# Kernel tuning notes

Measured on AMD Instinct MI355X. Metric: run time of the kernel, lower is better.

Reference implementation:

```python
import jax, jax.numpy as jnp
import numpy as np
from jax import lax

NPOINT = 1024
FG_NSAMPLE = 512
TOPK = 2048
NSAMPLE = 32
RADIUS = 0.3
BN_EPS = 1e-5


def masked_fps(xyz, mask, n):
    """Farthest point sampling restricted to points where mask is True.
    xyz: [B,N,3] (grad-stopped), mask: [B,N] bool. Returns int32 [B,n] indices.
    Equivalent to running FPS on the masked subset starting at its first point."""
    xyz = lax.stop_gradient(xyz)

    def one(x, m):
        mind0 = jnp.where(m, jnp.float32(1e10), jnp.float32(-1.0))

        def body(i, carry):
            mind, idxs = carry
            sel = jnp.argmax(mind).astype(jnp.int32)
            d = jnp.sum((x - x[sel]) ** 2, axis=-1)
            mind = jnp.where(m, jnp.minimum(mind, d), jnp.float32(-1.0))
            return mind, idxs.at[i].set(sel)

        _, idxs = lax.fori_loop(0, n, body, (mind0, jnp.zeros((n,), jnp.int32)))
        return idxs

    return jax.vmap(one)(xyz, mask)


def ball_query(xyz, new_xyz, radius, nsample):
    """xyz: [B,N,3], new_xyz: [B,S,3] -> int32 [B,S,nsample] of first neighbors
    within radius (padded with the first found index, as in pointnet2 CUDA)."""
    x = lax.stop_gradient(xyz)
    q = lax.stop_gradient(new_xyz)
    d2 = jnp.sum((q[:, :, None, :] - x[:, None, :, :]) ** 2, axis=-1)  # [B,S,N]
    N = x.shape[1]
    ar = jnp.arange(N, dtype=jnp.float32)
    key = jnp.where(d2 <= radius * radius, ar, jnp.float32(N))
    neg_top, _ = lax.top_k(-key, nsample)  # smallest nsample indices
    idx = (-neg_top).astype(jnp.int32)
    first = idx[..., :1]
    idx = jnp.where(idx >= N, first, idx)
    return jnp.clip(idx, 0, N - 1)


def conv_bn_relu_2d(x, W, g, b):
    # x: [B,C,S,ns], W: [O,C]; 1x1 conv (no bias) + training-mode BN + ReLU
    y = jnp.einsum('oc,bcsn->bosn', W, x)
    mu = y.mean((0, 2, 3), keepdims=True)
    var = y.var((0, 2, 3), keepdims=True)
    y = (y - mu) * lax.rsqrt(var + BN_EPS) * g[None, :, None, None] + b[None, :, None, None]
    return jax.nn.relu(y)


def conv_bn_relu_1d(x, W, g, b):
    # x: [B,C,N]
    y = jnp.einsum('oc,bcn->bon', W, x)
    mu = y.mean((0, 2), keepdims=True)
    var = y.var((0, 2), keepdims=True)
    y = (y - mu) * lax.rsqrt(var + BN_EPS) * g[None, :, None] + b[None, :, None]
    return jax.nn.relu(y)


def batch_gather_points(x, idx):
    # x: [B,N,3], idx: [B,...] -> [B,...,3]
    return jax.vmap(lambda a, i: a[i])(x, idx)


def batch_gather_feats(f, idx):
    # f: [B,C,N], idx: [B,S,ns] -> [B,C,S,ns]
    return jax.vmap(lambda a, i: a[:, i])(f, idx)


def setup_inputs() -> dict:
    key = jax.random.key(0)
    ks = jax.random.split(key, 16)
    B, N, C = 4, 16384, 128
    s = 0.05
    return {
        'xyz': jax.random.uniform(ks[0], (B, N, 3), dtype=jnp.float32),
        'features': jax.random.normal(ks[1], (B, C, N), dtype=jnp.float32),
        # grouped shared MLP: (3+C)->128->128->256
        'w1': jax.random.normal(ks[2], (128, 131), dtype=jnp.float32) * s,
        'g1': jnp.ones((128,), jnp.float32), 'b1': jnp.zeros((128,), jnp.float32),
        'w2': jax.random.normal(ks[3], (128, 128), dtype=jnp.float32) * s,
        'g2': jnp.ones((128,), jnp.float32), 'b2': jnp.zeros((128,), jnp.float32),
        'w3': jax.random.normal(ks[4], (256, 128), dtype=jnp.float32) * s,
        'g3': jnp.ones((256,), jnp.float32), 'b3': jnp.zeros((256,), jnp.float32),
        # fbs mask MLP: C->64->2 (last layer plain conv with bias)
        'fw1': jax.random.normal(ks[5], (64, 128), dtype=jnp.float32) * s,
        'fg1': jnp.ones((64,), jnp.float32), 'fb1': jnp.zeros((64,), jnp.float32),
        'fw2': jax.random.normal(ks[6], (2, 64), dtype=jnp.float32) * s,
        'fbias2': jnp.zeros((2,), jnp.float32),
    }


def reference(xyz, features, w1, g1, b1, w2, g2, b2, w3, g3, b3, fw1, fg1, fb1, fw2, fbias2):
    B, N, _ = xyz.shape
    # --- FBS: foreground/background scoring ---
    h = conv_bn_relu_1d(features, fw1, fg1, fb1)                 # [B,64,N]
    mask_scores = jnp.einsum('oc,bcn->bon', fw2, h) + fbias2[None, :, None]  # [B,2,N]
    soft = jax.nn.softmax(mask_scores, axis=1)
    margin = soft[:, 1, :] - soft[:, 0, :]                        # [B,N]
    _, top_idx = lax.top_k(margin, TOPK)
    fg_mask = jnp.zeros((B, N), bool).at[jnp.arange(B)[:, None], top_idx].set(True)
    # --- mask-restricted FPS on foreground and background ---
    fg_idx = masked_fps(xyz, fg_mask, FG_NSAMPLE)                 # [B,512]
    bg_idx = masked_fps(xyz, ~fg_mask, NPOINT - FG_NSAMPLE)       # [B,512]
    indices = jnp.concatenate([fg_idx, bg_idx], axis=1)          # [B,npoint]
    new_xyz = batch_gather_points(xyz, indices)                   # [B,npoint,3]
    # --- ball query + grouping ---
    idx = ball_query(xyz, new_xyz, RADIUS, NSAMPLE)               # [B,S,ns]
    grouped_xyz = batch_gather_points(xyz, idx)                   # [B,S,ns,3]
    grouped_xyz = grouped_xyz - new_xyz[:, :, None, :]
    grouped_xyz = jnp.transpose(grouped_xyz, (0, 3, 1, 2))        # [B,3,S,ns]
    grouped_feats = batch_gather_feats(features, idx)             # [B,C,S,ns]
    x = jnp.concatenate([grouped_xyz, grouped_feats], axis=1)     # [B,3+C,S,ns]
    # --- shared MLP + max pool over neighbors ---
    x = conv_bn_relu_2d(x, w1, g1, b1)
    x = conv_bn_relu_2d(x, w2, g2, b2)
    x = conv_bn_relu_2d(x, w3, g3, b3)
    new_features = jnp.max(x, axis=-1)                            # [B,256,S]
    return new_xyz, new_features, indices, mask_scores
```

## Files before the change

kernel.cpp:

```cpp
#include <hip/hip_runtime.h>

#define BB 4
#define NPT 16384
#define CIN 128
#define SS 1024
#define NS 32
#define PP 131072
#define TOPKK 2048

typedef unsigned short u16;
typedef unsigned int u32;
typedef unsigned long long u64;
typedef float v2 __attribute__((ext_vector_type(2)));
typedef short bf16x8 __attribute__((ext_vector_type(8)));
typedef float f32x4 __attribute__((ext_vector_type(4)));

__device__ __forceinline__ float bf2f(u32 v){ return __uint_as_float(v << 16); }
__device__ __forceinline__ u16 f2bf(float f){
  u32 u = __float_as_uint(f);
  u32 r = (u + 0x7FFFu + ((u >> 16) & 1u)) >> 16;
  return (u16)r;
}
__device__ __forceinline__ u32 keyOf(float m){
  u32 u = __float_as_uint(m);
  return (u & 0x80000000u) ? ~u : (u | 0x80000000u);
}

__device__ __forceinline__ float wave_max_f32(float v){
  #define STEP(CTRL) { int o_ = __builtin_amdgcn_update_dpp(0, __float_as_int(v), CTRL, 0xf, 0xf, true); \
                       v = fmaxf(v, __int_as_float(o_)); }
  STEP(0x111) STEP(0x112) STEP(0x114) STEP(0x118)
  STEP(0x142) STEP(0x143)
  #undef STEP
  return __int_as_float(__builtin_amdgcn_readlane(__float_as_int(v), 63));
}

#define OFF_NEWXYZ 0ull
#define OFF_MARGIN 49152ull
#define OFF_FGMASK 311296ull
#define OFF_IDXNB  573440ull
#define OFF_MSTAT  1097728ull
#define OFF_SSA    1098240ull
#define OFF_WT0    1104384ull
#define OFF_W1B    1137152ull
#define OFF_W2B    1178112ull
#define OFF_W3B    1210880ull
#define OFF_WT3F   1276416ull
#define OFF_MPART  1407488ull
#define OFF_CPART  2456064ull
#define OFF_REGB   10844672ull
#define OFF_REGA   44399104ull
#define WS_NEED    86342144ull

__global__ void k_prep(const float* __restrict__ w1, const float* __restrict__ w2,
                       const float* __restrict__ w3, const float* __restrict__ fw1,
                       float* __restrict__ wt0, u16* __restrict__ w1b, u16* __restrict__ w2b,
                       u16* __restrict__ w3b, float* __restrict__ wt3f){
  int gt = blockIdx.x*blockDim.x + threadIdx.x;
  int gs = gridDim.x*blockDim.x;
  for (int i = gt; i < 128*64;  i += gs){ int k=i>>6, m=i&63;  wt0[i] = fw1[m*128+k]; }
  for (int i = gt; i < 128*160; i += gs){ int m=i/160, k=i-m*160; w1b[i] = (k<131)? f2bf(w1[m*131+k]) : (u16)0; }
  for (int i = gt; i < 128*128; i += gs){ w2b[i] = f2bf(w2[i]); }
  for (int i = gt; i < 256*128; i += gs){ w3b[i] = f2bf(w3[i]); }
  for (int i = gt; i < 128*256; i += gs){ int k=i>>8, m=i&255; wt3f[i] = w3[m*128+k]; }
}

__global__ __launch_bounds__(256) void k_gemm_mask(const float* __restrict__ Wt,
                                                   const float* __restrict__ feat,
                                                   float* __restrict__ y0,
                                                   double* __restrict__ mpart){
  __shared__ float As[32][64];
  __shared__ float Bs[32][64];
  int t = threadIdx.x, tx = t & 15, ty = t >> 4;
  int p0 = blockIdx.x * 64; int b = blockIdx.z;
  const float* X = feat + (size_t)b * CIN * NPT;
  float acc[4][4] = {};
  int e = t * 8, ka = e >> 6, ca = e & 63;
  for (int kc = 0; kc < 4; kc++){
    const float* wr = Wt + (size_t)(kc*32 + ka) * 64 + ca;
    float4 w0 = *(const float4*)wr;
    float4 w1v = *(const float4*)(wr + 4);
    const float* br = X + (size_t)(kc*32 + ka) * NPT + p0 + ca;
    float4 b0 = *(const float4*)br;
    float4 b1 = *(const float4*)(br + 4);
    __syncthreads();
    *(float4*)&As[ka][ca] = w0; *(float4*)&As[ka][ca+4] = w1v;
    *(float4*)&Bs[ka][ca] = b0; *(float4*)&Bs[ka][ca+4] = b1;
    __syncthreads();
    #pragma unroll
    for (int k = 0; k < 32; k++){
      float4 a = *(float4*)&As[k][ty*4];
      float4 bq = *(float4*)&Bs[k][tx*4];
      float av[4] = {a.x,a.y,a.z,a.w}; float bw[4] = {bq.x,bq.y,bq.z,bq.w};
      #pragma unroll
      for (int i = 0; i < 4; i++)
        #pragma unroll
        for (int j = 0; j < 4; j++) acc[i][j] = fmaf(av[i], bw[j], acc[i][j]);
    }
  }
  #pragma unroll
  for (int i = 0; i < 4; i++){
    int m = ty*4 + i;
    float4 v = make_float4(acc[i][0], acc[i][1], acc[i][2], acc[i][3]);
    *(float4*)(y0 + ((size_t)(b*64 + m)) * NPT + p0 + tx*4) = v;
  }
  __syncthreads();
  float* red = (float*)As;
  #pragma unroll
  for (int i = 0; i < 4; i++){
    float s = 0.f, q = 0.f;
    #pragma unroll
    for (int j = 0; j < 4; j++){ s += acc[i][j]; q += acc[i][j]*acc[i][j]; }
    red[((ty*4+i)*16 + tx)*2] = s; red[((ty*4+i)*16 + tx)*2 + 1] = q;
  }
  __syncthreads();
  if (t < 64){
    double s = 0.0, q = 0.0;
    for (int x = 0; x < 16; x++){ s += red[(t*16+x)*2]; q += red[(t*16+x)*2+1]; }
    int slot = b*256 + blockIdx.x;
    mpart[((size_t)t*1024 + slot)*2] = s;
    mpart[((size_t)t*1024 + slot)*2 + 1] = q;
  }
}

__global__ void k_mask_stats(const double* __restrict__ mpart, float* __restrict__ mstat){
  int t = threadIdx.x;
  double s = 0.0, q = 0.0;
  for (int i = 0; i < 1024; i++){ s += mpart[((size_t)t*1024 + i)*2]; q += mpart[((size_t)t*1024 + i)*2+1]; }
  double cnt = 65536.0;
  double mu = s/cnt; double var = q/cnt - mu*mu;
  mstat[t*2] = (float)mu; mstat[t*2+1] = 1.0f / sqrtf((float)var + 1e-5f);
}

__global__ __launch_bounds__(256) void k_scores(const float* __restrict__ y0, const float* __restrict__ mstat,
                                                const float* __restrict__ fg1, const float* __restrict__ fb1,
                                                const float* __restrict__ fw2, const float* __restrict__ fbias2,
                                                float* __restrict__ margin, float* __restrict__ out3){
  __shared__ float smu[64], srs[64], sg[64], sb[64], sw[128];
  int t = threadIdx.x; int b = blockIdx.y; int n = blockIdx.x*256 + t;
  if (t < 64){ smu[t] = mstat[t*2]; srs[t] = mstat[t*2+1]; sg[t] = fg1[t]; sb[t] = fb1[t]; }
  if (t < 128) sw[t] = fw2[t];
  __syncthreads();
  float a0 = 0.f, a1 = 0.f;
  const float* yb = y0 + (size_t)b*64*NPT + n;
  for (int o = 0; o < 64; o++){
    float y = yb[(size_t)o * NPT];
    float h = __fmul_rn(__fmul_rn(__fsub_rn(y, smu[o]), srs[o]), sg[o]);
    h = __fadd_rn(h, sb[o]);
    h = fmaxf(h, 0.f);
    a0 = fmaf(sw[o], h, a0);
    a1 = fmaf(sw[64+o], h, a1);
  }
  float s0 = __fadd_rn(a0, fbias2[0]);
  float s1 = __fadd_rn(a1, fbias2[1]);
  out3[(size_t)(b*2)*NPT + n] = s0;
  out3[(size_t)(b*2+1)*NPT + n] = s1;
  float m = fmaxf(s0, s1);
  float e0 = expf(__fsub_rn(s0, m));
  float e1 = expf(__fsub_rn(s1, m));
  float den = __fadd_rn(e0, e1);
  margin[b*NPT + n] = __fsub_rn(__fdiv_rn(e1, den), __fdiv_rn(e0, den));
}

__global__ __launch_bounds__(1024) void k_topk(const float* __restrict__ margin, u32* __restrict__ fgmask){
  int t = threadIdx.x; int b = blockIdx.x;
  int lane = t & 63, wv = t >> 6;
  const float* mg = margin + b*NPT; u32* fm = fgmask + b*NPT;
  __shared__ int hist[256];
  __shared__ int swt[2][16];
  __shared__ u32 s_bin; __shared__ int s_need;
  int need = TOPKK; u32 prefix = 0, kmask = 0;
  for (int r = 0; r < 4; r++){
    int shift = 24 - 8*r;
    if (t < 256) hist[t] = 0;
    __syncthreads();
    for (int j = 0; j < 16; j++){
      u32 key = keyOf(mg[j*1024 + t]);
      if ((key & kmask) == prefix) atomicAdd(&hist[(key >> shift) & 255], 1);
    }
    __syncthreads();
    if (t == 0){
      int cum = 0;
      for (int bin = 255; bin >= 0; bin--){
        int c = hist[bin];
        if (cum + c >= need){ s_bin = (u32)bin; s_need = need - cum; break; }
        cum += c;
      }
    }
    __syncthreads();
    prefix |= s_bin << shift; kmask |= 255u << shift; need = s_need;
    __syncthreads();
  }
  u32 T = prefix;
  int run = 0;
  for (int j = 0; j < 16; j++){
    int n = j*1024 + t;
    u32 key = keyOf(mg[n]);
    int eq = (key == T) ? 1 : 0;
    int gt = (key > T) ? 1 : 0;
    u64 bal = __ballot(eq != 0);
    int lexcl = __popcll(bal & ((1ull << lane) - 1ull));
    if (lane == 0) swt[j & 1][wv] = __popcll(bal);
    __syncthreads();
    int base = 0, tot = 0;
    #pragma unroll
    for (int w = 0; w < 16; w++){
      int c = swt[j & 1][w];
      tot += c;
      if (w < wv) base += c;
    }
    int flag = gt | (eq & ((run + base + lexcl) < need ? 1 : 0));
    fm[n] = (u32)flag;
    run += tot;
  }
}

__global__ __launch_bounds__(1024) void k_compact(const float* __restrict__ xyz, const u32* __restrict__ fgmask,
                                                  float* __restrict__ cx, float* __restrict__ cy,
                                                  float* __restrict__ cz, int* __restrict__ cg){
  int blk = blockIdx.x; int b = blk >> 1; int which = blk & 1;
  const float* xb = xyz + (size_t)b * NPT * 3;
  const u32* mb = fgmask + b*NPT;
  int t = threadIdx.x;
  __shared__ int sc[1024];
  u32 mloc = 0; int cnt = 0;
  int p0 = t*16;
  #pragma unroll
  for (int j = 0; j < 16; j++){
    u32 m = mb[p0+j];
    bool inc = which ? (m == 0u) : (m != 0u);
    mloc |= (inc ? 1u : 0u) << j; cnt += inc ? 1 : 0;
  }
  sc[t] = cnt; __syncthreads();
  for (int off = 1; off < 1024; off <<= 1){
    int v = (t >= off) ? sc[t-off] : 0;
    __syncthreads();
    sc[t] += v;
    __syncthreads();
  }
  int pos = sc[t] - cnt;
  int base = b*16384 + (which ? 2048 : 0);
  for (int j = 0; j < 16; j++){
    if ((mloc >> j) & 1u){
      int p = p0 + j;
      cx[base+pos] = xb[p*3]; cy[base+pos] = xb[p*3+1]; cz[base+pos] = xb[p*3+2];
      cg[base+pos] = p; pos++;
    }
  }
}

template<int NV>
__device__ __forceinline__ void fps_run(const float* __restrict__ cx, const float* __restrict__ cy,
                                        const float* __restrict__ cz, const int* __restrict__ cg,
                                        int b, int which,
                                        float* __restrict__ newxyz, float* __restrict__ out0,
                                        float* __restrict__ out2){
  #pragma clang fp contract(off)
  int t = threadIdx.x;
  __shared__ u64 slots[2][8];
  if (t < 16) ((u64*)slots)[t] = 0ull;
  v2 px[NV], py[NV], pz[NV], mind[NV];
  #pragma unroll
  for (int r = 0; r < NV; r++){
    int p0 = 2048*r + t, p1 = 2048*r + 1024 + t;
    px[r].x = cx[p0]; px[r].y = cx[p1];
    py[r].x = cy[p0]; py[r].y = cy[p1];
    pz[r].x = cz[p0]; pz[r].y = cz[p1];
    mind[r].x = 1e10f; mind[r].y = 1e10f;
  }
  __syncthreads();
  float bv = 1e10f; int bi = t;
  for (int it = 0; it < 512; it++){
    float wall = wave_max_f32(bv);
    if (bv == wall){
      u64 key = ((u64)(it+1) << 46) | ((u64)keyOf(bv) << 14) | (u64)(16383 - bi);
      atomicMax((unsigned long long*)&slots[it & 1][t & 7], (unsigned long long)key);
    }
    __syncthreads();
    u64 k0 = slots[it & 1][0];
    #pragma unroll
    for (int i = 1; i < 8; i++){ u64 ki = slots[it & 1][i]; if (ki > k0) k0 = ki; }
    int sel = 16383 - (int)(k0 & 0x3FFFu);
    float xs = cx[sel], ys = cy[sel], zs = cz[sel];
    if (t == 0){
      int s = which*512 + it;
      out2[b*1024 + s] = (float)cg[sel];
      newxyz[(b*1024 + s)*3]   = xs;
      newxyz[(b*1024 + s)*3+1] = ys;
      newxyz[(b*1024 + s)*3+2] = zs;
      out0[(b*1024 + s)*3]   = xs;
      out0[(b*1024 + s)*3+1] = ys;
      out0[(b*1024 + s)*3+2] = zs;
    }
    v2 xs2; xs2.x = xs; xs2.y = xs;
    v2 ys2; ys2.x = ys; ys2.y = ys;
    v2 zs2; zs2.x = zs; zs2.y = zs;
    bv = -1.0f; bi = 16383;
    #pragma unroll
    for (int r = 0; r < NV; r++){
      v2 dx = px[r] - xs2;
      v2 dy = py[r] - ys2;
      v2 dz = pz[r] - zs2;
      v2 qx = dx * dx;
      v2 qy = dy * dy;
      v2 qz = dz * dz;
      v2 s1 = qx + qy;
      v2 d  = s1 + qz;
      float m0 = fminf(mind[r].x, d.x);
      float m1 = fminf(mind[r].y, d.y);
      mind[r].x = m0; mind[r].y = m1;
      if (m0 > bv){ bv = m0; bi = 2048*r + t; }
      if (m1 > bv){ bv = m1; bi = 2048*r + 1024 + t; }
    }
  }
}

__global__ __launch_bounds__(1024) void k_fps(const float* __restrict__ cx, const float* __restrict__ cy,
                                              const float* __restrict__ cz, const int* __restrict__ cg,
                                              float* __restrict__ newxyz, float* __restrict__ out0,
                                              float* __restrict__ out2){
  int b = blockIdx.x >> 1; int which = blockIdx.x & 1;
  int base = b*16384 + (which ? 2048 : 0);
  if (which) fps_run<7>(cx+base, cy+base, cz+base, cg+base, b, 1, newxyz, out0, out2);
  else       fps_run<1>(cx+base, cy+base, cz+base, cg+base, b, 0, newxyz, out0, out2);
}

__global__ __launch_bounds__(256) void k_ball(const float* __restrict__ xyz, const float* __restrict__ newxyz,
                                              int* __restrict__ idxnb){
  int t = threadIdx.x; int lane = t & 63;
  int qid = blockIdx.x*4 + (t >> 6);
  int b = qid >> 10;
  const float* xb = xyz + (size_t)b * NPT * 3;
  float qx = newxyz[qid*3], qy = newxyz[qid*3+1], qz = newxyz[qid*3+2];
  int found = 0, first = -1;
  for (int base = 0; base < NPT; base += 64){
    int p = base + lane;
    float x = xb[p*3], y = xb[p*3+1], z = xb[p*3+2];
    float dx = __fsub_rn(qx, x), dy = __fsub_rn(qy, y), dz = __fsub_rn(qz, z);
    float d2 = __fadd_rn(__fadd_rn(__fmul_rn(dx,dx), __fmul_rn(dy,dy)), __fmul_rn(dz,dz));
    bool w = d2 <= 0.09f;
    u64 m = __ballot(w);
    if (first < 0 && m) first = base + __ffsll((unsigned long long)m) - 1;
    if (w){
      int pos = found + __popcll(m & ((1ull << lane) - 1ull));
      if (pos < NS) idxnb[(size_t)qid*NS + pos] = p;
    }
    found += __popcll(m);
    if (found >= NS) break;
  }
  if (first < 0) first = 0;
  if (lane < NS && lane >= found) idxnb[(size_t)qid*NS + lane] = first;
}

__global__ __launch_bounds__(256) void k_buildX(const float* __restrict__ xyz, const float* __restrict__ newxyz,
                                                const int* __restrict__ idxnb, const float* __restrict__ feat,
                                                u16* __restrict__ Xb2){
  int pos = blockIdx.x*256 + threadIdx.x;
  int b = pos >> 15; int r = pos & 32767; int s = r >> 5;
  int gi = idxnb[pos] & (NPT - 1);
  const float* xp = xyz + ((size_t)b*NPT + gi) * 3;
  const float* qp = newxyz + ((size_t)(b << 10) + s) * 3;
  float dxyz[3];
  #pragma unroll
  for (int c = 0; c < 3; c++) dxyz[c] = __fsub_rn(xp[c], qp[c]);
  const float* fb = feat + (size_t)b*CIN*NPT + gi;
  for (int g8 = 0; g8 < 20; g8++){
    u32 pk[4];
    #pragma unroll
    for (int i = 0; i < 4; i++){
      u16 v0, v1;
      int c0 = g8*8 + 2*i, c1 = c0 + 1;
      float f0 = (c0 < 3) ? dxyz[c0] : ((c0 < 131) ? fb[(size_t)(c0-3)*NPT] : 0.f);
      float f1 = (c1 < 3) ? dxyz[c1] : ((c1 < 131) ? fb[(size_t)(c1-3)*NPT] : 0.f);
      v0 = f2bf(f0); v1 = f2bf(f1);
      pk[i] = (u32)v0 | ((u32)v1 << 16);
    }
    *(uint4*)(Xb2 + ((size_t)g8*PP + pos)*8) = make_uint4(pk[0], pk[1], pk[2], pk[3]);
  }
}

template<int NKS, int STORE>
__global__ __launch_bounds__(256) void k_mfma(const u16* __restrict__ Wb, int Kpad,
                                              const u16* __restrict__ Xp,
                                              u16* __restrict__ Yp, double* __restrict__ cpart){
  __shared__ float sred[4][16][16][2];
  int t = threadIdx.x;
  int w = t >> 6, lane = t & 63;
  int q = lane >> 4, c = lane & 15;
  int p0 = blockIdx.x * 64, m0 = blockIdx.y * 64;
  int m_w = m0 + w*16;
  f32x4 acc[4] = {{0.f,0.f,0.f,0.f},{0.f,0.f,0.f,0.f},{0.f,0.f,0.f,0.f},{0.f,0.f,0.f,0.f}};
  const u16* arow = Wb + (size_t)(m_w + c) * Kpad + q*8;
  #pragma unroll
  for (int ks = 0; ks < NKS; ks++){
    bf16x8 afrag = *(const bf16x8*)(arow + ks*32);
    #pragma unroll
    for (int pp = 0; pp < 4; pp++){
      int p = p0 + pp*16 + c;
      bf16x8 bfrag = *(const bf16x8*)(Xp + (((size_t)(ks*4 + q) * PP) + p) * 8);
      acc[pp] = __builtin_amdgcn_mfma_f32_16x16x32_bf16(afrag, bfrag, acc[pp], 0, 0, 0);
    }
  }
  #pragma unroll
  for (int reg = 0; reg < 4; reg++){
    float s = 0.f, sq = 0.f;
    #pragma unroll
    for (int pp = 0; pp < 4; pp++){ float v = acc[pp][reg]; s += v; sq += v*v; }
    sred[w][q*4+reg][c][0] = s; sred[w][q*4+reg][c][1] = sq;
  }
  if (STORE){
    int kgm = (m_w + q*4) >> 3;
    int j0 = (m_w + q*4) & 7;
    #pragma unroll
    for (int pp = 0; pp < 4; pp++){
      int p = p0 + pp*16 + c;
      ushort4 pk;
      pk.x = f2bf(acc[pp][0]); pk.y = f2bf(acc[pp][1]); pk.z = f2bf(acc[pp][2]); pk.w = f2bf(acc[pp][3]);
      *(ushort4*)(Yp + (((size_t)kgm * PP) + p) * 8 + j0) = pk;
    }
  }
  __syncthreads();
  if (t < 64){
    int ww = t >> 4, ml = t & 15;
    double s = 0.0, qq = 0.0;
    for (int cc = 0; cc < 16; cc++){ s += sred[ww][ml][cc][0]; qq += sred[ww][ml][cc][1]; }
    cpart[((size_t)(m0 + t) * 2048 + blockIdx.x)*2] = s;
    cpart[((size_t)(m0 + t) * 2048 + blockIdx.x)*2 + 1] = qq;
  }
}

__global__ __launch_bounds__(256) void k_stats_conv(const double* __restrict__ cpart,
                                                    const float* __restrict__ g, const float* __restrict__ bt,
                                                    float2* __restrict__ ssv){
  __shared__ double rs_[256], rq_[256];
  int ch = blockIdx.x, t = threadIdx.x;
  double s = 0.0, q = 0.0;
  for (int i = t; i < 2048; i += 256){ s += cpart[((size_t)ch*2048 + i)*2]; q += cpart[((size_t)ch*2048 + i)*2+1]; }
  rs_[t] = s; rq_[t] = q; __syncthreads();
  for (int off = 128; off; off >>= 1){
    if (t < off){ rs_[t] += rs_[t+off]; rq_[t] += rq_[t+off]; }
    __syncthreads();
  }
  if (t == 0){
    double cnt = (double)PP;
    double mu = rs_[0]/cnt; double var = rq_[0]/cnt - mu*mu;
    float rsf = 1.0f / sqrtf((float)var + 1e-5f);
    double rsd = (double)rsf;
    double gd = (double)g[ch]; double bd = (double)bt[ch];
    ssv[ch] = make_float2((float)(rsd*gd), (float)(bd - mu*rsd*gd));
  }
}

__global__ __launch_bounds__(256) void k_affine(u16* __restrict__ y, const float2* __restrict__ aff){
  int tid = blockIdx.x*256 + threadIdx.x;
  int kg = tid >> 17; int p = tid & (PP - 1);
  uint4* ptr = (uint4*)(y + (((size_t)kg*PP) + p)*8);
  uint4 u = *ptr;
  u32 us[4] = {u.x, u.y, u.z, u.w};
  u32 outp[4];
  #pragma unroll
  for (int i = 0; i < 4; i++){
    float2 a0 = aff[kg*8 + 2*i], a1 = aff[kg*8 + 2*i + 1];
    float v0 = fmaxf(0.f, fmaf(bf2f(us[i] & 0xFFFFu), a0.x, a0.y));
    float v1 = fmaxf(0.f, fmaf(bf2f(us[i] >> 16),     a1.x, a1.y));
    outp[i] = (u32)f2bf(v0) | ((u32)f2bf(v1) << 16);
  }
  *ptr = make_uint4(outp[0], outp[1], outp[2], outp[3]);
}

__global__ __launch_bounds__(256) void k_fuse3pool(const u16* __restrict__ Y2a, const float* __restrict__ wt3f,
                                                   const float2* __restrict__ ss2, float* __restrict__ out1){
  __shared__ float Xs[128*36];
  int t = threadIdx.x;
  int qid = blockIdx.x;
  int b = qid >> 10, s = qid & 1023;
  size_t cb = (size_t)qid << 5;
  #pragma unroll
  for (int e = 0; e < 2; e++){
    int lin = e*256 + t; int kg = lin >> 5, j = lin & 31;
    uint4 u = *(const uint4*)(Y2a + ((size_t)kg*PP + cb + j)*8);
    u32 us[4] = {u.x, u.y, u.z, u.w};
    #pragma unroll
    for (int i = 0; i < 4; i++){
      Xs[(kg*8 + 2*i    )*36 + j] = bf2f(us[i] & 0xFFFFu);
      Xs[(kg*8 + 2*i + 1)*36 + j] = bf2f(us[i] >> 16);
    }
  }
  __syncthreads();
  float acc[32] = {};
  for (int k = 0; k < 128; k++){
    float w = wt3f[k*256 + t];
    const float4* xr = (const float4*)&Xs[k*36];
    #pragma unroll
    for (int jq = 0; jq < 8; jq++){
      float4 x = xr[jq];
      acc[jq*4+0] = fmaf(w, x.x, acc[jq*4+0]);
      acc[jq*4+1] = fmaf(w, x.y, acc[jq*4+1]);
      acc[jq*4+2] = fmaf(w, x.z, acc[jq*4+2]);
      acc[jq*4+3] = fmaf(w, x.w, acc[jq*4+3]);
    }
  }
  float2 a2 = ss2[t];
  float mx = 0.f;
  #pragma unroll
  for (int j = 0; j < 32; j++) mx = fmaxf(mx, fmaxf(0.f, fmaf(acc[j], a2.x, a2.y)));
  out1[((size_t)b << 18) + (size_t)t*1024 + s] = mx;
}

extern "C" void kernel_launch(void* const* d_in, const int* in_sizes, int n_in,
                              void* d_out, int out_size, void* d_ws, size_t ws_size,
                              hipStream_t stream){
  (void)in_sizes; (void)n_in; (void)out_size;
  if (ws_size < WS_NEED) return;
  const float* xyz    = (const float*)d_in[0];
  const float* feat   = (const float*)d_in[1];
  const float* w1     = (const float*)d_in[2];
  const float* g1     = (const float*)d_in[3];
  const float* b1     = (const float*)d_in[4];
  const float* w2     = (const float*)d_in[5];
  const float* g2     = (const float*)d_in[6];
  const float* b2     = (const float*)d_in[7];
  const float* w3     = (const float*)d_in[8];
  const float* g3     = (const float*)d_in[9];
  const float* b3     = (const float*)d_in[10];
  const float* fw1    = (const float*)d_in[11];
  const float* fg1    = (const float*)d_in[12];
  const float* fb1    = (const float*)d_in[13];
  const float* fw2    = (const float*)d_in[14];
  const float* fbias2 = (const float*)d_in[15];

  char* ws = (char*)d_ws;
  float*  newxyz = (float*)(ws + OFF_NEWXYZ);
  float*  margin = (float*)(ws + OFF_MARGIN);
  u32*    fgmask = (u32*)(ws + OFF_FGMASK);
  int*    idxnb  = (int*)(ws + OFF_IDXNB);
  float*  mstat  = (float*)(ws + OFF_MSTAT);
  float2* ss0    = (float2*)(ws + OFF_SSA);
  float2* ss1    = ss0 + 128;
  float2* ss2    = ss0 + 256;
  float*  wt0    = (float*)(ws + OFF_WT0);
  u16*    w1b    = (u16*)(ws + OFF_W1B);
  u16*    w2b    = (u16*)(ws + OFF_W2B);
  u16*    w3b    = (u16*)(ws + OFF_W3B);
  float*  wt3f   = (float*)(ws + OFF_WT3F);
  double* mpart  = (double*)(ws + OFF_MPART);
  double* cpart  = (double*)(ws + OFF_CPART);
  u16*    Y1p    = (u16*)(ws + OFF_REGB);
  float*  y0     = (float*)(ws + OFF_REGA);
  float*  cx     = (float*)(ws + OFF_REGA);
  float*  cy     = cx + 4*16384;
  float*  cz     = cy + 4*16384;
  int*    cg     = (int*)(cz + 4*16384);
  u16*    Xb2    = (u16*)(ws + OFF_REGA);
  u16*    Y2p    = (u16*)(ws + OFF_REGA);

  float* out  = (float*)d_out;
  float* out0 = out;
  float* out1 = out + 12288;
  float* out2 = out + 1060864;
  float* out3 = out + 1064960;

  k_prep<<<dim3(256), dim3(256), 0, stream>>>(w1, w2, w3, fw1, wt0, w1b, w2b, w3b, wt3f);
  k_gemm_mask<<<dim3(256,1,4), dim3(256), 0, stream>>>(wt0, feat, y0, mpart);
  k_mask_stats<<<dim3(1), dim3(64), 0, stream>>>(mpart, mstat);
  k_scores<<<dim3(64,4), dim3(256), 0, stream>>>(y0, mstat, fg1, fb1, fw2, fbias2, margin, out3);
  k_topk<<<dim3(4), dim3(1024), 0, stream>>>(margin, fgmask);
  k_compact<<<dim3(8), dim3(1024), 0, stream>>>(xyz, fgmask, cx, cy, cz, cg);
  k_fps<<<dim3(8), dim3(1024), 0, stream>>>(cx, cy, cz, cg, newxyz, out0, out2);
  k_ball<<<dim3(1024), dim3(256), 0, stream>>>(xyz, newxyz, idxnb);
  k_buildX<<<dim3(512), dim3(256), 0, stream>>>(xyz, newxyz, idxnb, feat, Xb2);
  k_mfma<5,1><<<dim3(2048,2), dim3(256), 0, stream>>>(w1b, 160, Xb2, Y1p, cpart);
  k_stats_conv<<<dim3(128), dim3(256), 0, stream>>>(cpart, g1, b1, ss0);
  k_affine<<<dim3(8192), dim3(256), 0, stream>>>(Y1p, ss0);
  k_mfma<4,1><<<dim3(2048,2), dim3(256), 0, stream>>>(w2b, 128, Y1p, Y2p, cpart);
  k_stats_conv<<<dim3(128), dim3(256), 0, stream>>>(cpart, g2, b2, ss1);
  k_affine<<<dim3(8192), dim3(256), 0, stream>>>(Y2p, ss1);
  k_mfma<4,0><<<dim3(2048,4), dim3(256), 0, stream>>>(w3b, 128, Y2p, (u16*)nullptr, cpart);
  k_stats_conv<<<dim3(256), dim3(256), 0, stream>>>(cpart, g3, b3, ss2);
  k_fuse3pool<<<dim3(4096), dim3(256), 0, stream>>>(Y2p, wt3f, ss2, out1);
}
```

Measured before the change: 1.362 ms.

## Replace scalar fp32 conv3+pool with MFMA kernel and halve FPS block size

The final conv3 recompute plus max-pool, previously a scalar fp32 FMA kernel using a transposed fp32 weight copy, becomes a bf16 MFMA kernel that applies the BN affine and ReLU in registers and max-reduces over the 32 neighbors with DPP row reductions. The extra weight transpose in the prep kernel is dropped. Separately, the FPS kernel now runs with 512 threads per block and twice as many points per thread, which cuts barrier and wave-reduction overhead per iteration at the cost of more serial distance work per thread. The conv3 recompute now multiplies bf16 weights instead of fp32 weights, so the pooled output may differ slightly from before.

Result: faster. 1.233 ms (-9.5%).

```diff
diff --git a/kernel.cpp b/kernel.cpp
--- a/kernel.cpp
+++ b/kernel.cpp
@@ -33,6 +33,14 @@
   STEP(0x142) STEP(0x143)
   #undef STEP
   return __int_as_float(__builtin_amdgcn_readlane(__float_as_int(v), 63));
+}
+
+__device__ __forceinline__ float row_max16(float v){
+  #define STEP(CTRL) { int o_ = __builtin_amdgcn_update_dpp(0, __float_as_int(v), CTRL, 0xf, 0xf, true); \
+                       v = fmaxf(v, __int_as_float(o_)); }
+  STEP(0x111) STEP(0x112) STEP(0x114) STEP(0x118)
+  #undef STEP
+  return v;
 }
 
 #define OFF_NEWXYZ 0ull
@@ -45,7 +53,6 @@
 #define OFF_W1B    1137152ull
 #define OFF_W2B    1178112ull
 #define OFF_W3B    1210880ull
-#define OFF_WT3F   1276416ull
 #define OFF_MPART  1407488ull
 #define OFF_CPART  2456064ull
 #define OFF_REGB   10844672ull
@@ -55,14 +62,13 @@
 __global__ void k_prep(const float* __restrict__ w1, const float* __restrict__ w2,
                        const float* __restrict__ w3, const float* __restrict__ fw1,
                        float* __restrict__ wt0, u16* __restrict__ w1b, u16* __restrict__ w2b,
-                       u16* __restrict__ w3b, float* __restrict__ wt3f){
+                       u16* __restrict__ w3b){
   int gt = blockIdx.x*blockDim.x + threadIdx.x;
   int gs = gridDim.x*blockDim.x;
   for (int i = gt; i < 128*64;  i += gs){ int k=i>>6, m=i&63;  wt0[i] = fw1[m*128+k]; }
   for (int i = gt; i < 128*160; i += gs){ int m=i/160, k=i-m*160; w1b[i] = (k<131)? f2bf(w1[m*131+k]) : (u16)0; }
   for (int i = gt; i < 128*128; i += gs){ w2b[i] = f2bf(w2[i]); }
   for (int i = gt; i < 256*128; i += gs){ w3b[i] = f2bf(w3[i]); }
-  for (int i = gt; i < 128*256; i += gs){ int k=i>>8, m=i&255; wt3f[i] = w3[m*128+k]; }
 }
 
 __global__ __launch_bounds__(256) void k_gemm_mask(const float* __restrict__ Wt,
@@ -262,7 +268,7 @@
   v2 px[NV], py[NV], pz[NV], mind[NV];
   #pragma unroll
   for (int r = 0; r < NV; r++){
-    int p0 = 2048*r + t, p1 = 2048*r + 1024 + t;
+    int p0 = 1024*r + t, p1 = 1024*r + 512 + t;
     px[r].x = cx[p0]; px[r].y = cx[p1];
     py[r].x = cy[p0]; py[r].y = cy[p1];
     pz[r].x = cz[p0]; pz[r].y = cz[p1];
@@ -309,20 +315,20 @@
       float m0 = fminf(mind[r].x, d.x);
       float m1 = fminf(mind[r].y, d.y);
       mind[r].x = m0; mind[r].y = m1;
-      if (m0 > bv){ bv = m0; bi = 2048*r + t; }
-      if (m1 > bv){ bv = m1; bi = 2048*r + 1024 + t; }
-    }
-  }
-}
-
-__global__ __launch_bounds__(1024) void k_fps(const float* __restrict__ cx, const float* __restrict__ cy,
-                                              const float* __restrict__ cz, const int* __restrict__ cg,
-                                              float* __restrict__ newxyz, float* __restrict__ out0,
-                                              float* __restrict__ out2){
+      if (m0 > bv){ bv = m0; bi = 1024*r + t; }
+      if (m1 > bv){ bv = m1; bi = 1024*r + 512 + t; }
+    }
+  }
+}
+
+__global__ __launch_bounds__(512) void k_fps(const float* __restrict__ cx, const float* __restrict__ cy,
+                                             const float* __restrict__ cz, const int* __restrict__ cg,
+                                             float* __restrict__ newxyz, float* __restrict__ out0,
+                                             float* __restrict__ out2){
   int b = blockIdx.x >> 1; int which = blockIdx.x & 1;
   int base = b*16384 + (which ? 2048 : 0);
-  if (which) fps_run<7>(cx+base, cy+base, cz+base, cg+base, b, 1, newxyz, out0, out2);
-  else       fps_run<1>(cx+base, cy+base, cz+base, cg+base, b, 0, newxyz, out0, out2);
+  if (which) fps_run<14>(cx+base, cy+base, cz+base, cg+base, b, 1, newxyz, out0, out2);
+  else       fps_run<2 >(cx+base, cy+base, cz+base, cg+base, b, 0, newxyz, out0, out2);
 }
 
 __global__ __launch_bounds__(256) void k_ball(const float* __restrict__ xyz, const float* __restrict__ newxyz,
@@ -368,12 +374,10 @@
     u32 pk[4];
     #pragma unroll
     for (int i = 0; i < 4; i++){
-      u16 v0, v1;
       int c0 = g8*8 + 2*i, c1 = c0 + 1;
       float f0 = (c0 < 3) ? dxyz[c0] : ((c0 < 131) ? fb[(size_t)(c0-3)*NPT] : 0.f);
       float f1 = (c1 < 3) ? dxyz[c1] : ((c1 < 131) ? fb[(size_t)(c1-3)*NPT] : 0.f);
-      v0 = f2bf(f0); v1 = f2bf(f1);
-      pk[i] = (u32)v0 | ((u32)v1 << 16);
+      pk[i] = (u32)f2bf(f0) | ((u32)f2bf(f1) << 16);
     }
     *(uint4*)(Xb2 + ((size_t)g8*PP + pos)*8) = make_uint4(pk[0], pk[1], pk[2], pk[3]);
   }
@@ -429,6 +433,46 @@
   }
 }
 
+__global__ __launch_bounds__(256) void k_mfma_pool(const u16* __restrict__ Wb,
+                                                   const u16* __restrict__ Xp,
+                                                   const float2* __restrict__ ss2,
+                                                   float* __restrict__ out1){
+  int t = threadIdx.x;
+  int w = t >> 6, lane = t & 63;
+  int q = lane >> 4, c = lane & 15;
+  int p0 = blockIdx.x * 64, m0 = blockIdx.y * 64;
+  int m_w = m0 + w*16;
+  f32x4 acc[4] = {{0.f,0.f,0.f,0.f},{0.f,0.f,0.f,0.f},{0.f,0.f,0.f,0.f},{0.f,0.f,0.f,0.f}};
+  const u16* arow = Wb + (size_t)(m_w + c) * 128 + q*8;
+  #pragma unroll
+  for (int ks = 0; ks < 4; ks++){
+    bf16x8 afrag = *(const bf16x8*)(arow + ks*32);
+    #pragma unroll
+    for (int pp = 0; pp < 4; pp++){
+      int p = p0 + pp*16 + c;
+      bf16x8 bfrag = *(const bf16x8*)(Xp + (((size_t)(ks*4 + q) * PP) + p) * 8);
+      acc[pp] = __builtin_amdgcn_mfma_f32_16x16x32_bf16(afrag, bfrag, acc[pp], 0, 0, 0);
+    }
+  }
+  int qid0 = blockIdx.x*2;
+  #pragma unroll
+  for (int reg = 0; reg < 4; reg++){
+    int m = m_w + q*4 + reg;
+    float2 af = ss2[m];
+    float x0 = fmaxf(0.f, fmaf(acc[0][reg], af.x, af.y));
+    float x1 = fmaxf(0.f, fmaf(acc[1][reg], af.x, af.y));
+    float x2 = fmaxf(0.f, fmaf(acc[2][reg], af.x, af.y));
+    float x3 = fmaxf(0.f, fmaf(acc[3][reg], af.x, af.y));
+    float v0 = row_max16(fmaxf(x0, x1));
+    float v1 = row_max16(fmaxf(x2, x3));
+    if (c == 15){
+      int qa = qid0, qb = qid0 + 1;
+      out1[((size_t)(qa >> 10) << 18) + (size_t)m*1024 + (qa & 1023)] = v0;
+      out1[((size_t)(qb >> 10) << 18) + (size_t)m*1024 + (qb & 1023)] = v1;
+    }
+  }
+}
+
 __global__ __launch_bounds__(256) void k_stats_conv(const double* __restrict__ cpart,
                                                     const float* __restrict__ g, const float* __restrict__ bt,
                                                     float2* __restrict__ ssv){
@@ -466,45 +510,6 @@
     outp[i] = (u32)f2bf(v0) | ((u32)f2bf(v1) << 16);
   }
   *ptr = make_uint4(outp[0], outp[1], outp[2], outp[3]);
-}
-
-__global__ __launch_bounds__(256) void k_fuse3pool(const u16* __restrict__ Y2a, const float* __restrict__ wt3f,
-                                                   const float2* __restrict__ ss2, float* __restrict__ out1){
-  __shared__ float Xs[128*36];
-  int t = threadIdx.x;
-  int qid = blockIdx.x;
-  int b = qid >> 10, s = qid & 1023;
-  size_t cb = (size_t)qid << 5;
-  #pragma unroll
-  for (int e = 0; e < 2; e++){
-    int lin = e*256 + t; int kg = lin >> 5, j = lin & 31;
-    uint4 u = *(const uint4*)(Y2a + ((size_t)kg*PP + cb + j)*8);
-    u32 us[4] = {u.x, u.y, u.z, u.w};
-    #pragma unroll
-    for (int i = 0; i < 4; i++){
-      Xs[(kg*8 + 2*i    )*36 + j] = bf2f(us[i] & 0xFFFFu);
-      Xs[(kg*8 + 2*i + 1)*36 + j] = bf2f(us[i] >> 16);
-    }
-  }
-  __syncthreads();
-  float acc[32] = {};
-  for (int k = 0; k < 128; k++){
-    float w = wt3f[k*256 + t];
-    const float4* xr = (const float4*)&Xs[k*36];
-    #pragma unroll
-    for (int jq = 0; jq < 8; jq++){
-      float4 x = xr[jq];
-      acc[jq*4+0] = fmaf(w, x.x, acc[jq*4+0]);
-      acc[jq*4+1] = fmaf(w, x.y, acc[jq*4+1]);
-      acc[jq*4+2] = fmaf(w, x.z, acc[jq*4+2]);
-      acc[jq*4+3] = fmaf(w, x.w, acc[jq*4+3]);
-    }
-  }
-  float2 a2 = ss2[t];
-  float mx = 0.f;
-  #pragma unroll
-  for (int j = 0; j < 32; j++) mx = fmaxf(mx, fmaxf(0.f, fmaf(acc[j], a2.x, a2.y)));
-  out1[((size_t)b << 18) + (size_t)t*1024 + s] = mx;
 }
 
 extern "C" void kernel_launch(void* const* d_in, const int* in_sizes, int n_in,
@@ -542,7 +547,6 @@
   u16*    w1b    = (u16*)(ws + OFF_W1B);
   u16*    w2b    = (u16*)(ws + OFF_W2B);
   u16*    w3b    = (u16*)(ws + OFF_W3B);
-  float*  wt3f   = (float*)(ws + OFF_WT3F);
   double* mpart  = (double*)(ws + OFF_MPART);
   double* cpart  = (double*)(ws + OFF_CPART);
   u16*    Y1p    = (u16*)(ws + OFF_REGB);
@@ -560,13 +564,13 @@
   float* out2 = out + 1060864;
   float* out3 = out + 1064960;
 
-  k_prep<<<dim3(256), dim3(256), 0, stream>>>(w1, w2, w3, fw1, wt0, w1b, w2b, w3b, wt3f);
+  k_prep<<<dim3(256), dim3(256), 0, stream>>>(w1, w2, w3, fw1, wt0, w1b, w2b, w3b);
   k_gemm_mask<<<dim3(256,1,4), dim3(256), 0, stream>>>(wt0, feat, y0, mpart);
   k_mask_stats<<<dim3(1), dim3(64), 0, stream>>>(mpart, mstat);
   k_scores<<<dim3(64,4), dim3(256), 0, stream>>>(y0, mstat, fg1, fb1, fw2, fbias2, margin, out3);
   k_topk<<<dim3(4), dim3(1024), 0, stream>>>(margin, fgmask);
   k_compact<<<dim3(8), dim3(1024), 0, stream>>>(xyz, fgmask, cx, cy, cz, cg);
-  k_fps<<<dim3(8), dim3(1024), 0, stream>>>(cx, cy, cz, cg, newxyz, out0, out2);
+  k_fps<<<dim3(8), dim3(512), 0, stream>>>(cx, cy, cz, cg, newxyz, out0, out2);
   k_ball<<<dim3(1024), dim3(256), 0, stream>>>(xyz, newxyz, idxnb);
   k_buildX<<<dim3(512), dim3(256), 0, stream>>>(xyz, newxyz, idxnb, feat, Xb2);
   k_mfma<5,1><<<dim3(2048,2), dim3(256), 0, stream>>>(w1b, 160, Xb2, Y1p, cpart);
@@ -577,5 +581,5 @@
   k_affine<<<dim3(8192), dim3(256), 0, stream>>>(Y2p, ss1);
   k_mfma<4,0><<<dim3(2048,4), dim3(256), 0, stream>>>(w3b, 128, Y2p, (u16*)nullptr, cpart);
   k_stats_conv<<<dim3(256), dim3(256), 0, stream>>>(cpart, g3, b3, ss2);
-  k_fuse3pool<<<dim3(4096), dim3(256), 0, stream>>>(Y2p, wt3f, ss2, out1);
-}
+  k_mfma_pool<<<dim3(2048,4), dim3(256), 0, stream>>>(w3b, Y2p, ss2, out1);
+}
```
